# Kernel tuning notes

Measured on AMD Instinct MI355X. Metric: run time of the kernel, lower is better.

Reference implementation:

```python
import jax, jax.numpy as jnp
import numpy as np

N_NODES = 50000
N_EDGES = 800000
VOCAB = 4096          # node_emb_size
EMB_DIM = 128         # node_emb_dim
HIDDEN = 128          # hidden_dim -> layer1 out = 2*HIDDEN
N_POS = 1024


def gcn_conv(h, edge_index, W, b, n):
    """PyG GCNConv: lin -> add self loops -> sym-normalized scatter-add -> +bias."""
    h = h @ W                                   # [N, out]
    row, col = edge_index[0], edge_index[1]     # source, target
    loop = jnp.arange(n)
    row = jnp.concatenate([row, loop])
    col = jnp.concatenate([col, loop])
    deg = jax.ops.segment_sum(jnp.ones(row.shape[0], dtype=h.dtype), col, num_segments=n)
    dinv = jnp.where(deg > 0, jax.lax.rsqrt(deg), 0.0)
    norm = dinv[row] * dinv[col]                # [E+N]
    msg = h[row] * norm[:, None]                # gather + scale
    return jax.ops.segment_sum(msg, col, num_segments=n) + b


def setup_inputs() -> dict:
    key = jax.random.key(0)
    ks = jax.random.split(key, 10)
    x = jax.random.randint(ks[0], (N_NODES, 1), 0, VOCAB)
    edge_index = jax.random.randint(ks[1], (2, N_EDGES), 0, N_NODES)
    x_position = jax.random.randint(ks[2], (N_POS,), 0, N_NODES)
    # Embedding init: normal(0, emb_dim^-0.5) per initialize_parameters
    emb = jax.random.normal(ks[3], (VOCAB, EMB_DIM), jnp.float32) * EMB_DIM ** -0.5
    # GCN / linear weights (glorot-ish)
    W1 = jax.random.normal(ks[4], (EMB_DIM, 2 * HIDDEN), jnp.float32) * (EMB_DIM ** -0.5)
    b1 = jnp.zeros((2 * HIDDEN,), jnp.float32)
    W2 = jax.random.normal(ks[5], (2 * HIDDEN, HIDDEN), jnp.float32) * ((2 * HIDDEN) ** -0.5)
    b2 = jnp.zeros((HIDDEN,), jnp.float32)
    Wc = jax.random.normal(ks[6], (HIDDEN, VOCAB), jnp.float32) * (HIDDEN ** -0.5)
    bc = jnp.zeros((VOCAB,), jnp.float32)
    return {"x": x, "edge_index": edge_index, "x_position": x_position,
            "emb": emb, "W1": W1, "b1": b1, "W2": W2, "b2": b2, "Wc": Wc, "bc": bc}


def reference(x, edge_index, x_position, emb, W1, b1, W2, b2, Wc, bc):
    n = x.shape[0]
    h = emb[x[:, 0]]                                   # Embedding + squeeze(1)
    h = jax.nn.relu(gcn_conv(h, edge_index, W1, b1, n))
    z = gcn_conv(h, edge_index, W2, b2, n)             # [N, HIDDEN]
    logits = z @ Wc + bc                               # classifier over all nodes
    # embedding stage: mean of classified rows at x_position, keep dim 0
    return jnp.mean(logits[x_position], axis=0, keepdims=True)  # [1, VOCAB]
```

## Files before the change

### kernel.cpp

```cpp
#include <hip/hip_runtime.h>

constexpr int EMB  = 128;
constexpr int H1D  = 256;
constexpr int H2D  = 128;
constexpr int VOC  = 4096;
constexpr int NSL  = 32;
constexpr int RPB  = 4;
constexpr int KT   = 16;

constexpr int NRANGE = 8;
constexpr int TEAMS  = 128;
constexpr int RCAP   = 6400;
constexpr int HIST_B = NRANGE * TEAMS;
constexpr int GEMM_B = VOC / RPB;
constexpr int KB_GRID = HIST_B + GEMM_B;

__global__ void kA_init(int* count, unsigned int* flagbits, unsigned int* needw,
                        float* wagg, float* wsum, int* nflag, int* total,
                        const int* __restrict__ xpos,
                        int n, int nwords, int np) {
    int t = threadIdx.x;
    if (blockIdx.x == 0) {
        for (int i = t; i < nwords; i += 256) flagbits[i] = 0u;
        for (int i = t; i < n; i += 256) count[i] = 0;
        __syncthreads();
        for (int i = t; i < np; i += 256) {
            int v = xpos[i];
            atomicAdd(&count[v], 1);
            atomicOr(&flagbits[v >> 5], 1u << (v & 31));
        }
        if (t == 0) { *nflag = 0; *total = 0; }
    } else {
        const int stride = (gridDim.x - 1) * 256;
        const int i0 = (blockIdx.x - 1) * 256 + t;
        for (int i = i0; i < n; i += stride) wagg[i] = 0.0f;
        for (int i = i0; i < nwords; i += stride) needw[i] = 0u;
        for (int i = i0; i < NSL * H1D; i += stride) wsum[i] = 0.0f;
    }
}

__global__ __launch_bounds__(256) void kB_embW1_hist(
        const float* __restrict__ emb, const float* __restrict__ W1,
        float* __restrict__ embW1,
        const int* __restrict__ row, const int* __restrict__ col,
        const unsigned int* __restrict__ flagbits,
        unsigned short* __restrict__ cntp16, unsigned int* markw,
        int ne, int R, int sTeam) {
    __shared__ unsigned int sbuf[RCAP];
    int t = threadIdx.x;
    if (blockIdx.x < HIST_B) {
        int h     = blockIdx.x;
        int team  = h >> 3;
        int range = h & (NRANGE - 1);
        int base  = range * R;
        for (int i = t; i < R; i += 256) sbuf[i] = 0u;
        __syncthreads();
        int q  = (((ne + TEAMS - 1) / TEAMS) + 255) & ~255;
        int e0 = team * q;
        int e1 = min(ne, e0 + q);
        for (int e = e0 + t; e < e1; e += 256) {
            int c = col[e];
            unsigned int d = (unsigned int)(c - base);
            if (d < (unsigned int)R) {
                atomicAdd(&sbuf[d], 1u);
                if ((flagbits[c >> 5] >> (c & 31)) & 1u) {
                    int r = row[e];
                    atomicOr(&markw[r >> 5], 1u << (r & 31));
                }
            }
        }
        __syncthreads();
        unsigned short* outp = cntp16 + (size_t)team * sTeam + base;
        for (int i = t; i < R; i += 256) outp[i] = (unsigned short)sbuf[i];
    } else {
        float* sf = (float*)sbuf;
        float (*er)[EMB]  = (float (*)[EMB])sf;
        float (*w1t)[H1D] = (float (*)[H1D])(sf + RPB * EMB);
        int r0 = (blockIdx.x - HIST_B) * RPB;
        if (t < RPB * EMB / 4)
            ((float4*)er)[t] = ((const float4*)(emb + (size_t)r0 * EMB))[t];
        float acc[RPB];
#pragma unroll
        for (int rr = 0; rr < RPB; rr++) acc[rr] = 0.0f;
#pragma unroll
        for (int kt = 0; kt < EMB / KT; kt++) {
            __syncthreads();
            const float4* w4 = (const float4*)(W1 + (size_t)kt * KT * H1D);
#pragma unroll
            for (int i = 0; i < KT * H1D / 4 / 256; i++)
                ((float4*)w1t)[t + i * 256] = w4[t + i * 256];
            __syncthreads();
#pragma unroll
            for (int k2 = 0; k2 < KT; k2++) {
                float w = w1t[k2][t];
                int k = kt * KT + k2;
#pragma unroll
                for (int rr = 0; rr < RPB; rr++) acc[rr] += er[rr][k] * w;
            }
        }
#pragma unroll
        for (int rr = 0; rr < RPB; rr++)
            embW1[(size_t)(r0 + rr) * H1D + t] = acc[rr];
    }
}

__global__ void k_alloc(unsigned int* needw,
                        const unsigned int* __restrict__ flagbits,
                        const unsigned short* __restrict__ cntp16,
                        const int* __restrict__ count,
                        const int* __restrict__ x,
                        float* wagg, int* needlist, int* nflag, int* total,
                        int* offs, int* cursor, unsigned int* pkc, int* cnt,
                        int n, int sTeam) {
    int v = blockIdx.x * blockDim.x + threadIdx.x;
    int lane = threadIdx.x & 63;
    int cv = 0;
    bool need = false;
    if (v < n) {
        const unsigned short* cp = cntp16 + v;
#pragma unroll 8
        for (int tt = 0; tt < TEAMS; tt++) cv += cp[(size_t)tt * sTeam];
        cnt[v] = cv;
        pkc[v] = ((unsigned int)cv << 16) | (unsigned int)(x[v] & 0xFFFF);
        bool mark = (needw[v >> 5] >> (v & 31)) & 1u;
        bool flag = (flagbits[v >> 5] >> (v & 31)) & 1u;
        need = mark || flag;
        if (flag) wagg[v] = (float)count[v] / ((float)cv + 1.0f);
    }
    unsigned long long nm = __ballot(need);
    int wbase = (v & ~63) >> 5;
    if (lane == 0)  needw[wbase]     = (unsigned int)(nm & 0xffffffffu);
    if (lane == 32) needw[wbase + 1] = (unsigned int)(nm >> 32);
    int seg = need ? cv : 0;
    int incl = seg;
#pragma unroll
    for (int d = 1; d < 64; d <<= 1) {
        int t2 = __shfl_up(incl, d);
        if (lane >= d) incl += t2;
    }
    int excl = incl - seg;
    int wave_total = __shfl(incl, 63);
    int rank = __popcll(nm & ((1ull << lane) - 1));
    int wcnt = __popcll(nm);
    int base_id = 0, base_off = 0;
    if (lane == 0) {
        if (wcnt > 0)       base_id  = atomicAdd(nflag, wcnt);
        if (wave_total > 0) base_off = atomicAdd(total, wave_total);
    }
    base_id  = __shfl(base_id, 0);
    base_off = __shfl(base_off, 0);
    if (need) {
        needlist[base_id + rank] = v;
        int o = base_off + excl;
        offs[v] = o;
        cursor[v] = o;
    }
}

__global__ void k_scatter(const int* __restrict__ row, const int* __restrict__ col,
                          const unsigned int* __restrict__ needw,
                          const unsigned int* __restrict__ flagbits,
                          const int* __restrict__ count,
                          const unsigned int* __restrict__ pkc,
                          int* cursor, unsigned int* srow4, float* wagg, int ne) {
    int e = blockIdx.x * blockDim.x + threadIdx.x;
    if (e < ne) {
        int c = col[e];
        if ((needw[c >> 5] >> (c & 31)) & 1u) {
            int r = row[e];
            int pos = atomicAdd(&cursor[c], 1);
            unsigned int pr = pkc[r];
            srow4[pos] = pr;
            if ((flagbits[c >> 5] >> (c & 31)) & 1u) {
                float dr = rsqrtf((float)(pr >> 16) + 1.0f);
                float dc = rsqrtf((float)(pkc[c] >> 16) + 1.0f);
                atomicAdd(&wagg[r], (float)count[c] * dc * dr);
            }
        }
    }
}

__global__ void k_fconv(const int* __restrict__ needlist, const int* __restrict__ nneed_p,
                        const float* __restrict__ wagg, const int* __restrict__ x,
                        const unsigned int* __restrict__ srow4,
                        const int* __restrict__ offs, const int* __restrict__ cnt,
                        const float* __restrict__ embW1, const float* __restrict__ b1,
                        float* __restrict__ wsum) {
    int lane = threadIdx.x & 63;
    int wib  = threadIdx.x >> 6;
    int wid  = blockIdx.x * (blockDim.x >> 6) + wib;
    int nw   = gridDim.x * (blockDim.x >> 6);
    int nn   = *nneed_p;
    const float4* __restrict__ ew = (const float4*)embW1;
    float4 bfrag = ((const float4*)b1)[lane];
    float4 acc2 = {0.0f, 0.0f, 0.0f, 0.0f};

    for (int i = wid; i < nn; i += nw) {
        int v = needlist[i];
        int cv = cnt[v];
        float dv = rsqrtf((float)cv + 1.0f);
        float wa = wagg[v];
        float4 s = ew[(size_t)x[v] * 64 + lane];
        float w0 = dv * dv;
        float4 acc;
        acc.x = bfrag.x + w0 * s.x;
        acc.y = bfrag.y + w0 * s.y;
        acc.z = bfrag.z + w0 * s.z;
        acc.w = bfrag.w + w0 * s.w;
        int start = offs[v], m = cv;
        for (int base = 0; base < m; base += 64) {
            int mm = min(64, m - base);
            int xr = 0; float wr = 0.0f;
            if (lane < mm) {
                unsigned int pk2 = srow4[start + base + lane];
                xr = (int)(pk2 & 0xFFFFu);
                wr = rsqrtf((float)(pk2 >> 16) + 1.0f) * dv;
            }
            int e = 0;
            for (; e + 4 <= mm; e += 4) {
                int i0 = __shfl(xr, e),     i1 = __shfl(xr, e + 1);
                int i2 = __shfl(xr, e + 2), i3 = __shfl(xr, e + 3);
                float q0 = __shfl(wr, e),     q1 = __shfl(wr, e + 1);
                float q2 = __shfl(wr, e + 2), q3 = __shfl(wr, e + 3);
                float4 t0 = ew[(size_t)i0 * 64 + lane];
                float4 t1 = ew[(size_t)i1 * 64 + lane];
                float4 t2 = ew[(size_t)i2 * 64 + lane];
                float4 t3 = ew[(size_t)i3 * 64 + lane];
                acc.x += q0 * t0.x + q1 * t1.x + q2 * t2.x + q3 * t3.x;
                acc.y += q0 * t0.y + q1 * t1.y + q2 * t2.y + q3 * t3.y;
                acc.z += q0 * t0.z + q1 * t1.z + q2 * t2.z + q3 * t3.z;
                acc.w += q0 * t0.w + q1 * t1.w + q2 * t2.w + q3 * t3.w;
            }
            for (; e < mm; e++) {
                int i0 = __shfl(xr, e);
                float q0 = __shfl(wr, e);
                float4 t0 = ew[(size_t)i0 * 64 + lane];
                acc.x += q0 * t0.x;
                acc.y += q0 * t0.y;
                acc.z += q0 * t0.z;
                acc.w += q0 * t0.w;
            }
        }
        acc2.x += wa * fmaxf(acc.x, 0.0f);
        acc2.y += wa * fmaxf(acc.y, 0.0f);
        acc2.z += wa * fmaxf(acc.z, 0.0f);
        acc2.w += wa * fmaxf(acc.w, 0.0f);
    }

    __shared__ float red[4][H1D];
    red[wib][4 * lane + 0] = acc2.x;
    red[wib][4 * lane + 1] = acc2.y;
    red[wib][4 * lane + 2] = acc2.z;
    red[wib][4 * lane + 3] = acc2.w;
    __syncthreads();
    int t = threadIdx.x;
    float ssum = red[0][t] + red[1][t] + red[2][t] + red[3][t];
    atomicAdd(&wsum[(blockIdx.x & (NSL - 1)) * H1D + t], ssum);
}

__global__ void k_zout(const float* __restrict__ wsum, const float* __restrict__ W2,
                       const float* __restrict__ b2, const float* __restrict__ Wc,
                       const float* __restrict__ bc, float* __restrict__ out,
                       float inv_np) {
    __shared__ float ws[H1D];
    __shared__ float z[H2D];
    __shared__ float red[256];
    int t = threadIdx.x;
    float s = 0.0f;
#pragma unroll
    for (int c2 = 0; c2 < NSL; c2++) s += wsum[c2 * H1D + t];
    ws[t] = s;
    __syncthreads();
    if (t < H2D) {
        float acc = 0.0f;
#pragma unroll 8
        for (int k = 0; k < H1D; k++) acc += ws[k] * W2[k * H2D + t];
        z[t] = b2[t] + acc * inv_np;
    }
    __syncthreads();
    int c  = blockIdx.x * 16 + (t & 15);
    int js = t >> 4;
    float acc = 0.0f;
#pragma unroll
    for (int j = js * 8; j < js * 8 + 8; j++) acc += z[j] * Wc[(size_t)j * VOC + c];
    red[t] = acc;
    __syncthreads();
    if (t < 16) {
        int cc = blockIdx.x * 16 + t;
        float o = bc[cc];
#pragma unroll
        for (int ss = 0; ss < 16; ss++) o += red[ss * 16 + t];
        out[cc] = o;
    }
}

extern "C" void kernel_launch(void* const* d_in, const int* in_sizes, int n_in,
                              void* d_out, int out_size, void* d_ws, size_t ws_size,
                              hipStream_t stream) {
    const int n  = in_sizes[0];
    const int ne = in_sizes[1] / 2;
    const int np = in_sizes[2];

    const int*   x    = (const int*)d_in[0];
    const int*   ei   = (const int*)d_in[1];
    const int*   xpos = (const int*)d_in[2];
    const float* emb  = (const float*)d_in[3];
    const float* W1   = (const float*)d_in[4];
    const float* b1   = (const float*)d_in[5];
    const float* W2   = (const float*)d_in[6];
    const float* b2   = (const float*)d_in[7];
    const float* Wc   = (const float*)d_in[8];
    const float* bc   = (const float*)d_in[9];
    float*       out  = (float*)d_out;

    const int* row = ei;
    const int* col = ei + ne;

    char* p = (char*)d_ws;
    auto alloc = [&](size_t bytes) {
        char* r = p;
        p += (bytes + 255) & ~(size_t)255;
        return r;
    };
    const int nb     = (n + 255) / 256;
    const int neb    = (ne + 255) / 256;
    const int nwords = nb * 8;
    const int R      = (n + NRANGE - 1) / NRANGE;
    const int sTeam  = NRANGE * R;

    int*            cnt      = (int*)alloc((size_t)n * 4);
    int*            offs     = (int*)alloc((size_t)n * 4);
    int*            cursor   = (int*)alloc((size_t)n * 4);
    int*            count    = (int*)alloc((size_t)n * 4);
    int*            needlist = (int*)alloc((size_t)n * 4);
    unsigned int*   needw    = (unsigned int*)alloc((size_t)nwords * 4);
    unsigned int*   flagbits = (unsigned int*)alloc((size_t)nwords * 4);
    unsigned int*   srow4    = (unsigned int*)alloc((size_t)ne * 4);
    unsigned int*   pkc      = (unsigned int*)alloc((size_t)n * 4);
    unsigned short* cntp16   = (unsigned short*)alloc((size_t)TEAMS * sTeam * 2);
    int*            nflag    = (int*)alloc(256 * 4);
    int*            total    = (int*)alloc(256 * 4);
    float*          wagg     = (float*)alloc((size_t)n * 4);
    float*          embW1    = (float*)alloc((size_t)VOC * H1D * 4);
    float*          wsum     = (float*)alloc((size_t)NSL * H1D * 4);

    kA_init<<<nb, 256, 0, stream>>>(count, flagbits, needw, wagg, wsum,
                                    nflag, total, xpos, n, nwords, np);
    kB_embW1_hist<<<KB_GRID, 256, 0, stream>>>(emb, W1, embW1, row, col, flagbits,
                                               cntp16, needw, ne, R, sTeam);
    k_alloc<<<nb, 256, 0, stream>>>(needw, flagbits, cntp16, count, x, wagg,
                                    needlist, nflag, total, offs, cursor, pkc, cnt,
                                    n, sTeam);
    k_scatter<<<neb, 256, 0, stream>>>(row, col, needw, flagbits, count, pkc,
                                       cursor, srow4, wagg, ne);
    k_fconv<<<2048, 256, 0, stream>>>(needlist, nflag, wagg, x, srow4, offs, cnt,
                                      embW1, b1, wsum);
    k_zout<<<VOC / 16, 256, 0, stream>>>(wsum, W2, b2, Wc, bc, out, 1.0f / (float)np);
}
```

Measured before the change: 172.0 us.

## Replace global cursor atomics in scatter with per-team LDS cursors from histogram prefix

k_alloc now converts the per-team 16-bit histogram counts into exclusive prefix offsets in place. k_scatter is relaunched with one block per (team, node-range) pair, mirroring the histogram partition. Each block seeds shared-memory cursors from offs plus the team prefix and places its edges with LDS atomics instead of global atomics on a cursor array. The cost is that each block rescans its team's whole edge chunk and keeps only edges whose target falls in its node range, so edge reads are multiplied by NRANGE. It also depends on the scatter partition exactly matching the histogram's team/range split.

```diff
diff --git a/kernel.cpp b/kernel.cpp
--- a/kernel.cpp
+++ b/kernel.cpp
@@ -106,20 +106,26 @@
 
 __global__ void k_alloc(unsigned int* needw,
                         const unsigned int* __restrict__ flagbits,
-                        const unsigned short* __restrict__ cntp16,
+                        unsigned short* cntp16,
                         const int* __restrict__ count,
                         const int* __restrict__ x,
                         float* wagg, int* needlist, int* nflag, int* total,
-                        int* offs, int* cursor, unsigned int* pkc, int* cnt,
+                        int* offs, unsigned int* pkc, int* cnt,
                         int n, int sTeam) {
     int v = blockIdx.x * blockDim.x + threadIdx.x;
     int lane = threadIdx.x & 63;
     int cv = 0;
     bool need = false;
     if (v < n) {
-        const unsigned short* cp = cntp16 + v;
+        unsigned short pfx = 0;
 #pragma unroll 8
-        for (int tt = 0; tt < TEAMS; tt++) cv += cp[(size_t)tt * sTeam];
+        for (int tt = 0; tt < TEAMS; tt++) {
+            size_t idx = (size_t)tt * sTeam + v;
+            unsigned short cc = cntp16[idx];
+            cntp16[idx] = pfx;
+            pfx = (unsigned short)(pfx + cc);
+        }
+        cv = (int)pfx;
         cnt[v] = cv;
         pkc[v] = ((unsigned int)cv << 16) | (unsigned int)(x[v] & 0xFFFF);
         bool mark = (needw[v >> 5] >> (v & 31)) & 1u;
@@ -151,26 +157,40 @@
     base_off = __shfl(base_off, 0);
     if (need) {
         needlist[base_id + rank] = v;
-        int o = base_off + excl;
-        offs[v] = o;
-        cursor[v] = o;
-    }
-}
-
-__global__ void k_scatter(const int* __restrict__ row, const int* __restrict__ col,
-                          const unsigned int* __restrict__ needw,
-                          const unsigned int* __restrict__ flagbits,
-                          const int* __restrict__ count,
-                          const unsigned int* __restrict__ pkc,
-                          int* cursor, unsigned int* srow4, float* wagg, int ne) {
-    int e = blockIdx.x * blockDim.x + threadIdx.x;
-    if (e < ne) {
+        offs[v] = base_off + excl;
+    }
+}
+
+__global__ __launch_bounds__(256) void k_scatter(
+        const int* __restrict__ row, const int* __restrict__ col,
+        const unsigned int* __restrict__ needw,
+        const unsigned int* __restrict__ flagbits,
+        const int* __restrict__ count,
+        const unsigned int* __restrict__ pkc,
+        const int* __restrict__ offs,
+        const unsigned short* __restrict__ base16,
+        unsigned int* srow4, float* wagg, int ne, int R, int sTeam) {
+    __shared__ unsigned int pos[RCAP];
+    int t = threadIdx.x;
+    int h     = blockIdx.x;
+    int team  = h >> 3;
+    int range = h & (NRANGE - 1);
+    int base  = range * R;
+    const unsigned short* bp = base16 + (size_t)team * sTeam + base;
+    for (int i = t; i < R; i += 256)
+        pos[i] = (unsigned int)offs[base + i] + (unsigned int)bp[i];
+    __syncthreads();
+    int q  = (((ne + TEAMS - 1) / TEAMS) + 255) & ~255;
+    int e0 = team * q;
+    int e1 = min(ne, e0 + q);
+    for (int e = e0 + t; e < e1; e += 256) {
         int c = col[e];
-        if ((needw[c >> 5] >> (c & 31)) & 1u) {
+        unsigned int d = (unsigned int)(c - base);
+        if (d < (unsigned int)R && ((needw[c >> 5] >> (c & 31)) & 1u)) {
             int r = row[e];
-            int pos = atomicAdd(&cursor[c], 1);
+            unsigned int p2 = atomicAdd(&pos[d], 1u);
             unsigned int pr = pkc[r];
-            srow4[pos] = pr;
+            srow4[p2] = pr;
             if ((flagbits[c >> 5] >> (c & 31)) & 1u) {
                 float dr = rsqrtf((float)(pr >> 16) + 1.0f);
                 float dc = rsqrtf((float)(pkc[c] >> 16) + 1.0f);
@@ -323,14 +343,12 @@
         return r;
     };
     const int nb     = (n + 255) / 256;
-    const int neb    = (ne + 255) / 256;
     const int nwords = nb * 8;
     const int R      = (n + NRANGE - 1) / NRANGE;
     const int sTeam  = NRANGE * R;
 
     int*            cnt      = (int*)alloc((size_t)n * 4);
     int*            offs     = (int*)alloc((size_t)n * 4);
-    int*            cursor   = (int*)alloc((size_t)n * 4);
     int*            count    = (int*)alloc((size_t)n * 4);
     int*            needlist = (int*)alloc((size_t)n * 4);
     unsigned int*   needw    = (unsigned int*)alloc((size_t)nwords * 4);
@@ -349,10 +367,10 @@
     kB_embW1_hist<<<KB_GRID, 256, 0, stream>>>(emb, W1, embW1, row, col, flagbits,
                                                cntp16, needw, ne, R, sTeam);
     k_alloc<<<nb, 256, 0, stream>>>(needw, flagbits, cntp16, count, x, wagg,
-                                    needlist, nflag, total, offs, cursor, pkc, cnt,
+                                    needlist, nflag, total, offs, pkc, cnt,
                                     n, sTeam);
-    k_scatter<<<neb, 256, 0, stream>>>(row, col, needw, flagbits, count, pkc,
-                                       cursor, srow4, wagg, ne);
+    k_scatter<<<HIST_B, 256, 0, stream>>>(row, col, needw, flagbits, count, pkc,
+                                          offs, cntp16, srow4, wagg, ne, R, sTeam);
     k_fconv<<<2048, 256, 0, stream>>>(needlist, nflag, wagg, x, srow4, offs, cnt,
                                       embW1, b1, wsum);
     k_zout<<<VOC / 16, 256, 0, stream>>>(wsum, W2, b2, Wc, bc, out, 1.0f / (float)np);
```

New measurement: 198.1 us. +15.2%, slower.
